# Kernel tuning notes

Measured on AMD Instinct MI355X. Metric: run time of the kernel, lower is better.

## Reference

```python
import jax, jax.numpy as jnp
import numpy as np

B, T, N, C = 8, 16, 2048, 512


def setup_inputs() -> dict:
    key = jax.random.key(0)
    k1, k2, k3, k4, k5, k6 = jax.random.split(key, 6)
    return {
        "vd_s": jax.random.normal(k1, (B, T, C), dtype=jnp.float32),
        "vd_nodes": jax.random.normal(k2, (B, N, C), dtype=jnp.float32),
        # 1x1 conv weights initialized N(0, 0.01) as in the torch module
        "W1": jax.random.normal(k3, (C, C), dtype=jnp.float32) * 0.01,
        "b1": jax.random.normal(k4, (C,), dtype=jnp.float32) * 0.01,
        "W2": jax.random.normal(k5, (C, C), dtype=jnp.float32) * 0.01,
        "b2": jax.random.normal(k6, (C,), dtype=jnp.float32) * 0.01,
    }


def reference(vd_s, vd_nodes, W1, b1, W2, b2):
    # propagation_step = 1 (as in the original module)
    def per_graph(s, nodes):
        # s: [T, C] scene features, nodes: [N, C] node features
        out_scene = s.mean(axis=0)                     # [C]
        state = nodes                                  # [N, C]
        # 1x1 convs on [N, C, 1, 1] == per-node linear layers
        mat1 = state @ W1.T + b1                       # [N, C]
        mat2 = state @ W2.T + b2                       # [N, C]
        adj = mat1 @ mat2.T                            # [N, N]
        soft_adj = jax.nn.softmax(adj, axis=1)         # row-softmax (dim=1)
        new_state = soft_adj @ state + state           # message update + residual
        gp_out = new_state.mean(axis=0)                # [C]
        return jnp.concatenate([out_scene, gp_out], axis=0)  # [2C]

    return jax.vmap(per_graph)(vd_s, vd_nodes)         # [B, 2C]
```

## Files before the change

### kernel.cpp

```cpp
#include <hip/hip_runtime.h>

typedef __bf16 bf16;
typedef __bf16 bf16x8 __attribute__((ext_vector_type(8), aligned(16)));
typedef float  f32x4  __attribute__((ext_vector_type(4)));
typedef float  f32x2  __attribute__((ext_vector_type(2)));
typedef long   longx2 __attribute__((ext_vector_type(2)));

#define B_ 8
#define T_ 16
#define N_ 2048
#define C_ 512

__device__ inline void gload_lds16(const void* g, void* l) {
    __builtin_amdgcn_global_load_lds(
        (const __attribute__((address_space(1))) void*)g,
        (__attribute__((address_space(3))) void*)l, 16, 0, 0);
}

__device__ inline unsigned char f32_to_fp8(float v) {
    int p = __builtin_amdgcn_cvt_pk_fp8_f32(v, 0.f, 0, false);
    return (unsigned char)(p & 0xff);
}

__device__ inline void fp8x4_to_f32(unsigned int wd, float* o) {
    f32x2 lo = __builtin_amdgcn_cvt_pk_f32_fp8((int)wd, false);
    f32x2 hi = __builtin_amdgcn_cvt_pk_f32_fp8((int)wd, true);
    o[0] = lo[0]; o[1] = lo[1]; o[2] = hi[0]; o[3] = hi[1];
}


__global__ __launch_bounds__(256) void k_prep(
    const float* __restrict__ vd_s, const float* __restrict__ nodes,
    const float* __restrict__ W1, const float* __restrict__ W2,
    float* __restrict__ out, bf16* __restrict__ nodes_bf,
    unsigned char* __restrict__ nodes_f8,
    bf16* __restrict__ W1t, bf16* __restrict__ W2t) {
    __shared__ float sh[32 * 33];
    const int bx = blockIdx.x, tid = threadIdx.x;
    if (bx < 2048) {
        size_t i = ((size_t)bx * 256 + tid) * 16;
        float v[16];
        *(float4*)&v[0]  = *(const float4*)(nodes + i);
        *(float4*)&v[4]  = *(const float4*)(nodes + i + 4);
        *(float4*)&v[8]  = *(const float4*)(nodes + i + 8);
        *(float4*)&v[12] = *(const float4*)(nodes + i + 12);
        bf16x8 b0, b1;
#pragma unroll
        for (int e = 0; e < 8; ++e) { b0[e] = (bf16)v[e]; b1[e] = (bf16)v[8 + e]; }
        *(bf16x8*)(nodes_bf + i)     = b0;
        *(bf16x8*)(nodes_bf + i + 8) = b1;
        unsigned int wds[4];
#pragma unroll
        for (int k = 0; k < 4; ++k) {
            int p = __builtin_amdgcn_cvt_pk_fp8_f32(v[k * 4 + 0], v[k * 4 + 1], 0, false);
            p = __builtin_amdgcn_cvt_pk_fp8_f32(v[k * 4 + 2], v[k * 4 + 3], p, true);
            wds[k] = (unsigned int)p;
        }
        int j = (int)((i >> 4) & 3);
        size_t base = i & ~(size_t)63;
        size_t pa1 = base + (size_t)(((2 * j) & 3) * 16 + (j >> 1) * 8);
        size_t pa2 = base + (size_t)(((2 * j + 1) & 3) * 16 + (j >> 1) * 8);
        uint2 u1; u1.x = wds[0]; u1.y = wds[1];
        uint2 u2; u2.x = wds[2]; u2.y = wds[3];
        *(uint2*)(nodes_f8 + pa1) = u1;
        *(uint2*)(nodes_f8 + pa2) = u2;
    } else if (bx < 2064) {
        int gt = (bx - 2048) * 256 + tid;
        int b = gt >> 9, c = gt & 511;
        float s = 0.f;
#pragma unroll
        for (int t = 0; t < T_; ++t) s += vd_s[(size_t)b * T_ * C_ + t * C_ + c];
        out[b * 2 * C_ + c] = s * (1.0f / T_);
    } else {
        const float* W = (bx < 2320) ? W1 : W2;
        bf16* Wt = (bx < 2320) ? W1t : W2t;
        int idx = (bx < 2320) ? bx - 2064 : bx - 2320;
        int bxx = (idx & 15) * 32, byy = (idx >> 4) * 32;
        int tx = tid & 31, ty = tid >> 5;
#pragma unroll
        for (int r = 0; r < 32; r += 8)
            sh[(ty + r) * 33 + tx] = W[(size_t)(byy + ty + r) * C_ + bxx + tx];
        __syncthreads();
#pragma unroll
        for (int r = 0; r < 32; r += 8)
            Wt[(size_t)(bxx + ty + r) * C_ + byy + tx] = (bf16)sh[tx * 33 + ty + r];
    }
}

__global__ void k_q(const float* __restrict__ b1, const bf16* __restrict__ W2t,
                    float* __restrict__ q) {
    int wid = threadIdx.x >> 6, lane = threadIdx.x & 63;
    int c = blockIdx.x * 4 + wid;
    bf16x8 v8 = *(const bf16x8*)(W2t + (size_t)c * C_ + lane * 8);
    float s = 0.f;
#pragma unroll
    for (int i = 0; i < 8; ++i) s += (float)v8[i] * b1[lane * 8 + i];
#pragma unroll
    for (int m = 32; m; m >>= 1) s += __shfl_xor(s, m);
    if (lane == 0) q[c] = s;
}

template <int OM>
__global__ __launch_bounds__(256) void gemm_nt(
    const bf16* __restrict__ A, size_t strideA,
    const bf16* __restrict__ Bm, size_t strideB,
    const float* __restrict__ bias,
    void* __restrict__ Cv, size_t strideC,
    int N, int K) {
    __shared__ __attribute__((aligned(16))) bf16 lA[128 * 64];
    __shared__ __attribute__((aligned(16))) bf16 lB[128 * 64];
    const int tid = threadIdx.x;
    const int lane = tid & 63, w = tid >> 6;
    const int wm = w >> 1, wn = w & 1;
    const int z = blockIdx.z;
    const int bm = blockIdx.x * 128, bn = blockIdx.y * 128;
    const bf16* Ab = A + (size_t)z * strideA;
    const bf16* Bb = Bm + (size_t)z * strideB;

    f32x4 acc[4][4];
#pragma unroll
    for (int i = 0; i < 4; ++i)
#pragma unroll
        for (int j = 0; j < 4; ++j) acc[i][j] = f32x4{0.f, 0.f, 0.f, 0.f};

    const int nkt = K >> 6;
    for (int kt = 0; kt < nkt; ++kt) {
#pragma unroll
        for (int c = 0; c < 4; ++c) {
            int ca = c * 256 + tid;
            int row = ca >> 3;
            int qd = (ca & 7) ^ (row & 7);
            gload_lds16(Ab + (size_t)(bm + row) * K + kt * 64 + qd * 8,
                        lA + c * 2048 + w * 512);
            gload_lds16(Bb + (size_t)(bn + row) * K + kt * 64 + qd * 8,
                        lB + c * 2048 + w * 512);
        }
        __syncthreads();

        bf16x8 af[2][4], bfr[2][4];
#pragma unroll
        for (int ks = 0; ks < 2; ++ks) {
            int y = ks * 4 + (lane >> 4);
#pragma unroll
            for (int i = 0; i < 4; ++i) {
                int ra = wm * 64 + i * 16 + (lane & 15);
                int rb = wn * 64 + i * 16 + (lane & 15);
                af[ks][i]  = *(const bf16x8*)&lA[ra * 64 + ((y ^ (ra & 7)) * 8)];
                bfr[ks][i] = *(const bf16x8*)&lB[rb * 64 + ((y ^ (rb & 7)) * 8)];
            }
        }
#pragma unroll
        for (int ks = 0; ks < 2; ++ks)
#pragma unroll
            for (int i = 0; i < 4; ++i)
#pragma unroll
                for (int j = 0; j < 4; ++j)
                    acc[i][j] = __builtin_amdgcn_mfma_f32_16x16x32_bf16(
                        af[ks][i], bfr[ks][j], acc[i][j], 0, 0, 0);
        __syncthreads();
    }

#pragma unroll
    for (int i = 0; i < 4; ++i) {
#pragma unroll
        for (int j = 0; j < 4; ++j) {
            int col = bn + wn * 64 + j * 16 + (lane & 15);
            float bv = bias ? bias[col] : 0.f;
#pragma unroll
            for (int r = 0; r < 4; ++r) {
                int row = bm + wm * 64 + i * 16 + (lane >> 4) * 4 + r;
                float v = acc[i][j][r] + bv;
                if constexpr (OM == 0) {
                    ((bf16*)Cv)[(size_t)z * strideC + (size_t)row * N + col] = (bf16)v;
                } else {
                    int m = lane & 15;
                    int colp = (col & ~63) + ((2 * j + (m >> 3)) & 3) * 16 +
                               (j >> 1) * 8 + (m & 7);
                    ((unsigned char*)Cv)[(size_t)z * strideC + (size_t)row * N + colp] =
                        f32_to_fp8(v * 16.0f);
                }
            }
        }
    }
}

__global__ __launch_bounds__(1024, 4) void gemm256w(
    const unsigned char* __restrict__ A, const unsigned char* __restrict__ Bm,
    unsigned char* __restrict__ P) {
    __shared__ __attribute__((aligned(16))) unsigned char ls[2][2][16384];
    const int tid = threadIdx.x;
    const int lane = tid & 63, w = tid >> 6;
    const int wm = w >> 2, wn = w & 3;
    const int q4 = lane >> 4;
    const int id = blockIdx.x;
    const int sw = (id & 7) * 64 + (id >> 3);
    const int z = sw >> 6, tt = sw & 63;
    const int bm = (tt >> 3) * 256, bn = (tt & 7) * 256;
    const unsigned char* Ab = A + (size_t)z * N_ * C_;
    const unsigned char* Bb = Bm + (size_t)z * N_ * C_;

    f32x4 acc[4][4];
#pragma unroll
    for (int i = 0; i < 4; ++i)
#pragma unroll
        for (int j = 0; j < 4; ++j) acc[i][j] = f32x4{0.f, 0.f, 0.f, 0.f};

#define STAGE_T(kt_, buf_)                                                        \
    {                                                                             \
        int row = tid >> 2;                                                       \
        int qd = (tid & 3) ^ (row & 3);                                           \
        gload_lds16(Ab + (size_t)(bm + row) * 512 + (kt_) * 64 + qd * 16,         \
                    &ls[buf_][0][w * 1024]);                                      \
        gload_lds16(Bb + (size_t)(bn + row) * 512 + (kt_) * 64 + qd * 16,         \
                    &ls[buf_][1][w * 1024]);                                      \
    }

    STAGE_T(0, 0);
    STAGE_T(1, 1);
    asm volatile("s_waitcnt vmcnt(2)" ::: "memory");
    __builtin_amdgcn_s_barrier();
    asm volatile("" ::: "memory");

#pragma unroll
    for (int j = 0; j < 8; ++j) {
        const int cur = j & 1;
        const unsigned char* lA = &ls[cur][0][0];
        const unsigned char* lB = &ls[cur][1][0];

        long af[4][2], bfv[4][2];
#pragma unroll
        for (int i = 0; i < 4; ++i) {
            int ra = wm * 64 + i * 16 + (lane & 15);
            longx2 t = *(const longx2*)&lA[ra * 64 + ((q4 ^ (ra & 3)) * 16)];
            af[i][0] = t[0]; af[i][1] = t[1];
        }
#pragma unroll
        for (int jj = 0; jj < 4; ++jj) {
            int rb = wn * 64 + jj * 16 + (lane & 15);
            longx2 t = *(const longx2*)&lB[rb * 64 + ((q4 ^ (rb & 3)) * 16)];
            bfv[jj][0] = t[0]; bfv[jj][1] = t[1];
        }
        __builtin_amdgcn_s_setprio(1);
#pragma unroll
        for (int ks = 0; ks < 2; ++ks)
#pragma unroll
            for (int i = 0; i < 4; ++i)
#pragma unroll
                for (int jj = 0; jj < 4; ++jj)
                    acc[i][jj] = __builtin_amdgcn_mfma_f32_16x16x32_fp8_fp8(
                        af[i][ks], bfv[jj][ks], acc[i][jj], 0, 0, 0);
        __builtin_amdgcn_s_setprio(0);

        asm volatile("" ::: "memory");
        __builtin_amdgcn_s_barrier();
        asm volatile("" ::: "memory");

        if (j + 2 < 8) STAGE_T(j + 2, cur);
        if (j < 7) {
            if (j < 6) asm volatile("s_waitcnt vmcnt(2)" ::: "memory");
            else       asm volatile("s_waitcnt vmcnt(0)" ::: "memory");
            __builtin_amdgcn_s_barrier();
            asm volatile("" ::: "memory");
        }
    }

    unsigned char* Pb = P + (size_t)z * N_ * N_;
#pragma unroll
    for (int fi = 0; fi < 4; ++fi) {
#pragma unroll
        for (int fj = 0; fj < 4; ++fj) {
            int col = bn + wn * 64 + fj * 16 + (lane & 15);
#pragma unroll
            for (int r = 0; r < 4; ++r) {
                int row = bm + wm * 64 + fi * 16 + (lane >> 4) * 4 + r;
                float v = __expf(fminf(acc[fi][fj][r] * 0.0625f, 8.8f)) * 0.0625f;
                Pb[(size_t)row * N_ + col] = f32_to_fp8(v);
            }
        }
    }
#undef STAGE_T
}

__global__ __launch_bounds__(256) void k_w2(const unsigned char* __restrict__ P,
                                            float* __restrict__ wpart) {
    __shared__ float rp[16 * 256];
    __shared__ float ri[16];
    const int tid = threadIdx.x;
    const int s = blockIdx.x, b = blockIdx.y;
    const unsigned char* Pb = P + (size_t)b * N_ * N_ + (size_t)s * 16 * N_;
    const int j0 = tid * 8;
    uint2 v[16];
#pragma unroll
    for (int r = 0; r < 16; ++r) {
        v[r] = *(const uint2*)&Pb[(size_t)r * N_ + j0];
        float f[8];
        fp8x4_to_f32(v[r].x, &f[0]);
        fp8x4_to_f32(v[r].y, &f[4]);
        float t = 0.f;
#pragma unroll
        for (int e = 0; e < 8; ++e) t += f[e];
        rp[r * 256 + tid] = t;
    }
    __syncthreads();
    {
        int row = tid >> 4, seg = tid & 15;
        float t = 0.f;
#pragma unroll
        for (int k = 0; k < 16; ++k) t += rp[row * 256 + seg + 16 * k];
#pragma unroll
        for (int m = 8; m; m >>= 1) t += __shfl_xor(t, m);
        if (seg == 0) ri[row] = 1.0f / t;
    }
    __syncthreads();
    float acc8[8] = {0.f, 0.f, 0.f, 0.f, 0.f, 0.f, 0.f, 0.f};
#pragma unroll
    for (int r = 0; r < 16; ++r) {
        float rr = ri[r];
        float f[8];
        fp8x4_to_f32(v[r].x, &f[0]);
        fp8x4_to_f32(v[r].y, &f[4]);
#pragma unroll
        for (int e = 0; e < 8; ++e) acc8[e] += rr * f[e];
    }
    float* wp = wpart + ((size_t)b * 128 + s) * (size_t)N_;
#pragma unroll
    for (int e = 0; e < 8; ++e) wp[j0 + e] = acc8[e];
}

__global__ __launch_bounds__(256) void k_gp(const unsigned char* __restrict__ nodes_f8,
                                            const float* __restrict__ wpart,
                                            float* __restrict__ gppart) {
    __shared__ float wred[4][64];
    __shared__ float wsh[64];
    __shared__ float gred[4][512];
    const int tid = threadIdx.x;
    const int slab = blockIdx.x, b = blockIdx.y;
    const int jj = tid & 63, sg = tid >> 6;
    float wacc = 0.f;
    for (int s = sg; s < 128; s += 4)
        wacc += wpart[((size_t)b * 128 + s) * N_ + slab * 64 + jj];
    wred[sg][jj] = wacc;
    __syncthreads();
    if (tid < 64)
        wsh[tid] = wred[0][tid] + wred[1][tid] + wred[2][tid] + wred[3][tid] + 1.0f;
    __syncthreads();
    const int j0 = slab * 64;
    const int cc = (tid & 63) * 8, jr = tid >> 6;
    const int lc = (cc & ~63) + ((cc >> 3) & 1) * 32 + ((cc >> 4) & 3) * 8;
    const unsigned char* nb = nodes_f8 + (size_t)b * N_ * C_;
    float acc8[8] = {0.f, 0.f, 0.f, 0.f, 0.f, 0.f, 0.f, 0.f};
    for (int j = jr; j < 64; j += 4) {
        float wj = wsh[j];
        uint2 nv = *(const uint2*)&nb[(size_t)(j0 + j) * C_ + cc];
        float f[8];
        fp8x4_to_f32(nv.x, &f[0]);
        fp8x4_to_f32(nv.y, &f[4]);
#pragma unroll
        for (int e = 0; e < 8; ++e) acc8[e] += wj * f[e];
    }
#pragma unroll
    for (int e = 0; e < 8; ++e) gred[jr][lc + e] = acc8[e];
    __syncthreads();
    if (tid < 64) {
#pragma unroll
        for (int e = 0; e < 8; ++e) {
            int c = tid * 8 + e;
            gppart[((size_t)slab * 8 + b) * C_ + c] =
                gred[0][c] + gred[1][c] + gred[2][c] + gred[3][c];
        }
    }
}

__global__ void k_fin(const float* __restrict__ gppart, float* __restrict__ out) {
    int gt = blockIdx.x * 256 + threadIdx.x;
    int b = gt >> 9, c = gt & 511;
    float s = 0.f;
#pragma unroll
    for (int k = 0; k < 32; ++k) s += gppart[((size_t)k * 8 + b) * C_ + c];
    out[b * 2 * C_ + C_ + c] = s * (1.0f / N_);
}

extern "C" void kernel_launch(void* const* d_in, const int* in_sizes, int n_in,
                              void* d_out, int out_size, void* d_ws, size_t ws_size,
                              hipStream_t stream) {
    const float* vd_s  = (const float*)d_in[0];
    const float* nodes = (const float*)d_in[1];
    const float* W1    = (const float*)d_in[2];
    const float* b1    = (const float*)d_in[3];
    const float* W2    = (const float*)d_in[4];
    float* out = (float*)d_out;

    char* ws = (char*)d_ws;
    bf16*          nodes_bf = (bf16*)(ws);
    unsigned char* H2f8     = (unsigned char*)(ws + ((size_t)16 << 20));
    float*         wpart    = (float*)(ws + ((size_t)16 << 20));
    unsigned char* nodes_f8 = (unsigned char*)(ws + ((size_t)24 << 20));
    unsigned char* P        = (unsigned char*)(ws + ((size_t)32 << 20));
    bf16*          W1t      = (bf16*)(ws + ((size_t)96 << 20));
    bf16*          W2t      = (bf16*)(ws + ((size_t)96 << 20) + (512u << 10));
    bf16*          Gt       = (bf16*)(ws + ((size_t)96 << 20) + (1024u << 10));
    char*          fbase    = ws + ((size_t)96 << 20) + (1536u << 10);
    float*         q        = (float*)(fbase);
    float*         gppart   = (float*)(fbase + 4096);

    k_prep<<<2576, 256, 0, stream>>>(vd_s, nodes, W1, W2,
                                     out, nodes_bf, nodes_f8, W1t, W2t);
    k_q<<<128, 256, 0, stream>>>(b1, W2t, q);

    gemm_nt<0><<<dim3(4, 4, 1), 256, 0, stream>>>(
        W2t, 0, W1t, 0, nullptr, Gt, 0, C_, C_);
    gemm_nt<1><<<dim3(16, 4, 8), 256, 0, stream>>>(
        nodes_bf, (size_t)N_ * C_, Gt, 0, q,
        H2f8, (size_t)N_ * C_, C_, C_);
    gemm256w<<<512, 1024, 0, stream>>>(H2f8, nodes_f8, P);

    k_w2<<<dim3(128, 8), 256, 0, stream>>>(P, wpart);
    k_gp<<<dim3(32, 8), 256, 0, stream>>>(nodes_f8, wpart, gppart);
    k_fin<<<16, 256, 0, stream>>>(gppart, out);
}
```

Baseline: 106.7 us.

## Fold q computation into prep kernel, drop final reduction kernel via atomics

```diff
diff --git a/kernel.cpp b/kernel.cpp
--- a/kernel.cpp
+++ b/kernel.cpp
@@ -32,9 +32,11 @@
 __global__ __launch_bounds__(256) void k_prep(
     const float* __restrict__ vd_s, const float* __restrict__ nodes,
     const float* __restrict__ W1, const float* __restrict__ W2,
+    const float* __restrict__ b1,
     float* __restrict__ out, bf16* __restrict__ nodes_bf,
     unsigned char* __restrict__ nodes_f8,
-    bf16* __restrict__ W1t, bf16* __restrict__ W2t) {
+    bf16* __restrict__ W1t, bf16* __restrict__ W2t,
+    float* __restrict__ qpart) {
     __shared__ float sh[32 * 33];
     const int bx = blockIdx.x, tid = threadIdx.x;
     if (bx < 2048) {
@@ -44,11 +46,11 @@
         *(float4*)&v[4]  = *(const float4*)(nodes + i + 4);
         *(float4*)&v[8]  = *(const float4*)(nodes + i + 8);
         *(float4*)&v[12] = *(const float4*)(nodes + i + 12);
-        bf16x8 b0, b1;
-#pragma unroll
-        for (int e = 0; e < 8; ++e) { b0[e] = (bf16)v[e]; b1[e] = (bf16)v[8 + e]; }
+        bf16x8 b0, b1v;
+#pragma unroll
+        for (int e = 0; e < 8; ++e) { b0[e] = (bf16)v[e]; b1v[e] = (bf16)v[8 + e]; }
         *(bf16x8*)(nodes_bf + i)     = b0;
-        *(bf16x8*)(nodes_bf + i + 8) = b1;
+        *(bf16x8*)(nodes_bf + i + 8) = b1v;
         unsigned int wds[4];
 #pragma unroll
         for (int k = 0; k < 4; ++k) {
@@ -71,7 +73,7 @@
 #pragma unroll
         for (int t = 0; t < T_; ++t) s += vd_s[(size_t)b * T_ * C_ + t * C_ + c];
         out[b * 2 * C_ + c] = s * (1.0f / T_);
-    } else {
+    } else if (bx < 2576) {
         const float* W = (bx < 2320) ? W1 : W2;
         bf16* Wt = (bx < 2320) ? W1t : W2t;
         int idx = (bx < 2320) ? bx - 2064 : bx - 2320;
@@ -84,27 +86,33 @@
 #pragma unroll
         for (int r = 0; r < 32; r += 8)
             Wt[(size_t)(bxx + ty + r) * C_ + byy + tx] = (bf16)sh[tx * 33 + ty + r];
-    }
-}
-
-__global__ void k_q(const float* __restrict__ b1, const bf16* __restrict__ W2t,
-                    float* __restrict__ q) {
-    int wid = threadIdx.x >> 6, lane = threadIdx.x & 63;
-    int c = blockIdx.x * 4 + wid;
-    bf16x8 v8 = *(const bf16x8*)(W2t + (size_t)c * C_ + lane * 8);
-    float s = 0.f;
-#pragma unroll
-    for (int i = 0; i < 8; ++i) s += (float)v8[i] * b1[lane * 8 + i];
-#pragma unroll
-    for (int m = 32; m; m >>= 1) s += __shfl_xor(s, m);
-    if (lane == 0) q[c] = s;
+    } else if (bx < 2592) {
+        int p = bx - 2576;
+#pragma unroll
+        for (int h = 0; h < 2; ++h) {
+            int c = h * 256 + tid;
+            float s = 0.f;
+#pragma unroll
+            for (int kk = 0; kk < 32; ++kk) {
+                int k = p * 32 + kk;
+                s += b1[k] * W2[(size_t)k * C_ + c];
+            }
+            qpart[p * 512 + c] = s;
+        }
+    } else {
+#pragma unroll
+        for (int r = 0; r < 16; ++r) {
+            int i = r * 256 + tid;
+            out[(i >> 9) * 2 * C_ + C_ + (i & 511)] = 0.f;
+        }
+    }
 }
 
 template <int OM>
 __global__ __launch_bounds__(256) void gemm_nt(
     const bf16* __restrict__ A, size_t strideA,
     const bf16* __restrict__ Bm, size_t strideB,
-    const float* __restrict__ bias,
+    const float* __restrict__ qpart,
     void* __restrict__ Cv, size_t strideC,
     int N, int K) {
     __shared__ __attribute__((aligned(16))) bf16 lA[128 * 64];
@@ -160,16 +168,25 @@
         __syncthreads();
     }
 
+    float bvj[4];
+#pragma unroll
+    for (int j = 0; j < 4; ++j) {
+        bvj[j] = 0.f;
+        if constexpr (OM == 1) {
+            int col = bn + wn * 64 + j * 16 + (lane & 15);
+#pragma unroll
+            for (int p = 0; p < 16; ++p) bvj[j] += qpart[p * 512 + col];
+        }
+    }
 #pragma unroll
     for (int i = 0; i < 4; ++i) {
 #pragma unroll
         for (int j = 0; j < 4; ++j) {
             int col = bn + wn * 64 + j * 16 + (lane & 15);
-            float bv = bias ? bias[col] : 0.f;
 #pragma unroll
             for (int r = 0; r < 4; ++r) {
                 int row = bm + wm * 64 + i * 16 + (lane >> 4) * 4 + r;
-                float v = acc[i][j][r] + bv;
+                float v = acc[i][j][r] + bvj[j];
                 if constexpr (OM == 0) {
                     ((bf16*)Cv)[(size_t)z * strideC + (size_t)row * N + col] = (bf16)v;
                 } else {
@@ -283,15 +300,15 @@
 
 __global__ __launch_bounds__(256) void k_w2(const unsigned char* __restrict__ P,
                                             float* __restrict__ wpart) {
-    __shared__ float rp[16 * 256];
-    __shared__ float ri[16];
+    __shared__ float rp[32 * 256];
+    __shared__ float ri[32];
     const int tid = threadIdx.x;
     const int s = blockIdx.x, b = blockIdx.y;
-    const unsigned char* Pb = P + (size_t)b * N_ * N_ + (size_t)s * 16 * N_;
+    const unsigned char* Pb = P + (size_t)b * N_ * N_ + (size_t)s * 32 * N_;
     const int j0 = tid * 8;
-    uint2 v[16];
-#pragma unroll
-    for (int r = 0; r < 16; ++r) {
+    uint2 v[32];
+#pragma unroll
+    for (int r = 0; r < 32; ++r) {
         v[r] = *(const uint2*)&Pb[(size_t)r * N_ + j0];
         float f[8];
         fp8x4_to_f32(v[r].x, &f[0]);
@@ -303,18 +320,18 @@
     }
     __syncthreads();
     {
-        int row = tid >> 4, seg = tid & 15;
+        int row = tid >> 3, seg = tid & 7;
         float t = 0.f;
 #pragma unroll
-        for (int k = 0; k < 16; ++k) t += rp[row * 256 + seg + 16 * k];
-#pragma unroll
-        for (int m = 8; m; m >>= 1) t += __shfl_xor(t, m);
+        for (int k = 0; k < 32; ++k) t += rp[row * 256 + seg + 8 * k];
+#pragma unroll
+        for (int m = 4; m; m >>= 1) t += __shfl_xor(t, m);
         if (seg == 0) ri[row] = 1.0f / t;
     }
     __syncthreads();
     float acc8[8] = {0.f, 0.f, 0.f, 0.f, 0.f, 0.f, 0.f, 0.f};
 #pragma unroll
-    for (int r = 0; r < 16; ++r) {
+    for (int r = 0; r < 32; ++r) {
         float rr = ri[r];
         float f[8];
         fp8x4_to_f32(v[r].x, &f[0]);
@@ -322,34 +339,31 @@
 #pragma unroll
         for (int e = 0; e < 8; ++e) acc8[e] += rr * f[e];
     }
-    float* wp = wpart + ((size_t)b * 128 + s) * (size_t)N_;
+    float* wp = wpart + ((size_t)b * 64 + s) * (size_t)N_;
 #pragma unroll
     for (int e = 0; e < 8; ++e) wp[j0 + e] = acc8[e];
 }
 
 __global__ __launch_bounds__(256) void k_gp(const unsigned char* __restrict__ nodes_f8,
                                             const float* __restrict__ wpart,
-                                            float* __restrict__ gppart) {
-    __shared__ float wred[4][64];
-    __shared__ float wsh[64];
+                                            float* __restrict__ out) {
+    __shared__ float wsh[256];
     __shared__ float gred[4][512];
     const int tid = threadIdx.x;
     const int slab = blockIdx.x, b = blockIdx.y;
-    const int jj = tid & 63, sg = tid >> 6;
-    float wacc = 0.f;
-    for (int s = sg; s < 128; s += 4)
-        wacc += wpart[((size_t)b * 128 + s) * N_ + slab * 64 + jj];
-    wred[sg][jj] = wacc;
+    const int j0 = slab * 256;
+    {
+        float wacc = 1.0f;
+        for (int s = 0; s < 64; ++s)
+            wacc += wpart[((size_t)b * 64 + s) * N_ + j0 + tid];
+        wsh[tid] = wacc;
+    }
     __syncthreads();
-    if (tid < 64)
-        wsh[tid] = wred[0][tid] + wred[1][tid] + wred[2][tid] + wred[3][tid] + 1.0f;
-    __syncthreads();
-    const int j0 = slab * 64;
     const int cc = (tid & 63) * 8, jr = tid >> 6;
     const int lc = (cc & ~63) + ((cc >> 3) & 1) * 32 + ((cc >> 4) & 3) * 8;
     const unsigned char* nb = nodes_f8 + (size_t)b * N_ * C_;
     float acc8[8] = {0.f, 0.f, 0.f, 0.f, 0.f, 0.f, 0.f, 0.f};
-    for (int j = jr; j < 64; j += 4) {
+    for (int j = jr; j < 256; j += 4) {
         float wj = wsh[j];
         uint2 nv = *(const uint2*)&nb[(size_t)(j0 + j) * C_ + cc];
         float f[8];
@@ -365,19 +379,10 @@
 #pragma unroll
         for (int e = 0; e < 8; ++e) {
             int c = tid * 8 + e;
-            gppart[((size_t)slab * 8 + b) * C_ + c] =
-                gred[0][c] + gred[1][c] + gred[2][c] + gred[3][c];
-        }
-    }
-}
-
-__global__ void k_fin(const float* __restrict__ gppart, float* __restrict__ out) {
-    int gt = blockIdx.x * 256 + threadIdx.x;
-    int b = gt >> 9, c = gt & 511;
-    float s = 0.f;
-#pragma unroll
-    for (int k = 0; k < 32; ++k) s += gppart[((size_t)k * 8 + b) * C_ + c];
-    out[b * 2 * C_ + C_ + c] = s * (1.0f / N_);
+            float s = gred[0][c] + gred[1][c] + gred[2][c] + gred[3][c];
+            atomicAdd(&out[b * 2 * C_ + C_ + c], s * (1.0f / N_));
+        }
+    }
 }
 
 extern "C" void kernel_launch(void* const* d_in, const int* in_sizes, int n_in,
@@ -399,22 +404,18 @@
     bf16*          W1t      = (bf16*)(ws + ((size_t)96 << 20));
     bf16*          W2t      = (bf16*)(ws + ((size_t)96 << 20) + (512u << 10));
     bf16*          Gt       = (bf16*)(ws + ((size_t)96 << 20) + (1024u << 10));
-    char*          fbase    = ws + ((size_t)96 << 20) + (1536u << 10);
-    float*         q        = (float*)(fbase);
-    float*         gppart   = (float*)(fbase + 4096);
-
-    k_prep<<<2576, 256, 0, stream>>>(vd_s, nodes, W1, W2,
-                                     out, nodes_bf, nodes_f8, W1t, W2t);
-    k_q<<<128, 256, 0, stream>>>(b1, W2t, q);
+    float*         qpart    = (float*)(ws + ((size_t)96 << 20) + (1536u << 10));
+
+    k_prep<<<2593, 256, 0, stream>>>(vd_s, nodes, W1, W2, b1,
+                                     out, nodes_bf, nodes_f8, W1t, W2t, qpart);
 
     gemm_nt<0><<<dim3(4, 4, 1), 256, 0, stream>>>(
         W2t, 0, W1t, 0, nullptr, Gt, 0, C_, C_);
     gemm_nt<1><<<dim3(16, 4, 8), 256, 0, stream>>>(
-        nodes_bf, (size_t)N_ * C_, Gt, 0, q,
+        nodes_bf, (size_t)N_ * C_, Gt, 0, qpart,
         H2f8, (size_t)N_ * C_, C_, C_);
     gemm256w<<<512, 1024, 0, stream>>>(H2f8, nodes_f8, P);
 
-    k_w2<<<dim3(128, 8), 256, 0, stream>>>(P, wpart);
-    k_gp<<<dim3(32, 8), 256, 0, stream>>>(nodes_f8, wpart, gppart);
-    k_fin<<<16, 256, 0, stream>>>(gppart, out);
-}
+    k_w2<<<dim3(64, 8), 256, 0, stream>>>(P, wpart);
+    k_gp<<<dim3(8, 8), 256, 0, stream>>>(nodes_f8, wpart, out);
+}
```

New measurement: 117.8 us. 10.4% more time.
